# Performance work log

Measured on AMD Instinct MI355X. Metric: run time of the kernel, lower is better.

The kernel has to match this reference:

```python
import jax, jax.numpy as jnp
import numpy as np

# dims
T, B, D = 128, 512, 512          # seq, batch, d_input = dim_aug_state*n_agent
M, H, DH, DFF = 6, 2, 32, 64     # mem_len, heads, d_head_inner, d_ff_inner
ACT = 64                          # dim_action*n_agent
BG = 0.1                          # GRU-gate bias (GTrXL)


def _ln(t, g, b):
    mu = t.mean(-1, keepdims=True)
    var = ((t - mu) ** 2).mean(-1, keepdims=True)
    return (t - mu) / jnp.sqrt(var + 1e-5) * g + b


def _rel_shift(x):
    # x: [T, J, B, H] -> TransformerXL relative shift
    Tq, J = x.shape[0], x.shape[1]
    zp = jnp.zeros((Tq, 1) + x.shape[2:], x.dtype)
    x = jnp.concatenate([zp, x], axis=1)              # [T, J+1, B, H]
    x = x.reshape((J + 1, Tq) + x.shape[2:])[1:]      # [J, T, B, H]
    return x.reshape((Tq, J) + x.shape[2:])


def _gate(x, y, W, b):
    # GRU-style gating g(x, y): x = residual stream, y = new branch output
    lin = lambda t, i: t @ W[i] + b[i]
    r = jax.nn.sigmoid(lin(y, 0) + lin(x, 1))
    z = jax.nn.sigmoid(lin(y, 2) + lin(x, 3) - BG)
    h = jnp.tanh(lin(y, 4) + (r * x) @ W[5] + b[5])
    return (1.0 - z) * x + z * h


def setup_inputs() -> dict:
    key = jax.random.key(0)
    ks = iter(jax.random.split(key, 32))
    rn = lambda shape, s=0.02: jax.random.normal(next(ks), shape, jnp.float32) * s
    return dict(
        aug_states=jax.random.normal(next(ks), (T, B, D), jnp.float32),
        action=jax.random.normal(next(ks), (B, ACT), jnp.float32),
        memory=jnp.zeros((M, B, D), jnp.float32),
        W_q=rn((D, H * DH)), W_kv=rn((D, 2 * H * DH)), W_p=rn((D, H * DH)), W_out=rn((H * DH, D)),
        u=rn((H, DH)), v=rn((H, DH)),
        ln1_g=jnp.ones(D), ln1_b=jnp.zeros(D), ln2_g=jnp.ones(D), ln2_b=jnp.zeros(D),
        ff_W1=rn((D, DFF)), ff_b1=jnp.zeros(DFF), ff_W2=rn((DFF, D)), ff_b2=jnp.zeros(D),
        g1_W=rn((6, D, D)), g1_b=jnp.zeros((6, D)), g2_W=rn((6, D, D)), g2_b=jnp.zeros((6, D)),
        d1_W=rn((D, 1024)), d1_b=jnp.zeros(1024),
        d2_W=rn((1024 + ACT, 512)), d2_b=jnp.zeros(512),
        d3_W=rn((512, 300)), d3_b=jnp.zeros(300),
        d4_W=rn((300, 1)), d4_b=jnp.zeros(1),
    )


def reference(aug_states, action, memory, W_q, W_kv, W_p, W_out, u, v,
              ln1_g, ln1_b, ln2_g, ln2_b, ff_W1, ff_b1, ff_W2, ff_b2,
              g1_W, g1_b, g2_W, g2_b, d1_W, d1_b, d2_W, d2_b, d3_W, d3_b, d4_W, d4_b):
    x = aug_states                                    # [T, B, D]
    J = T + M
    # sinusoidal relative position embeddings for positions J-1 .. 0
    pos = jnp.arange(J - 1, -1, -1.0, dtype=jnp.float32)
    inv_freq = 1.0 / (10000.0 ** (jnp.arange(0, D, 2, dtype=jnp.float32) / D))
    si = pos[:, None] * inv_freq[None, :]
    pos_emb = jnp.concatenate([jnp.sin(si), jnp.cos(si)], axis=-1)   # [J, D]

    # --- stable (pre-LN + gated) TransformerXL layer ---
    src2 = _ln(x, ln1_g, ln1_b)
    cat = jnp.concatenate([memory, src2], axis=0)     # [J, B, D]
    k, vv = jnp.split(cat @ W_kv, 2, axis=-1)
    q = (src2 @ W_q).reshape(T, B, H, DH)
    k = k.reshape(J, B, H, DH)
    vv = vv.reshape(J, B, H, DH)
    p = (pos_emb @ W_p).reshape(J, H, DH)
    content = jnp.einsum("ibhd,jbhd->ijbh", q + u, k)
    position = _rel_shift(jnp.einsum("ibhd,jhd->ijbh", q + v, p))
    attn = content + position                         # [T, J, B, H]
    mask = jnp.arange(J)[None, :] > (jnp.arange(T)[:, None] + M)     # causal w/ memory offset
    attn = jnp.where(mask[:, :, None, None], -jnp.inf, attn)
    attn = jax.nn.softmax(attn * (1.0 / np.sqrt(DH)), axis=1)
    av = jnp.einsum("ijbh,jbhd->ibhd", attn, vv).reshape(T, B, H * DH)
    src = _gate(x, av @ W_out, g1_W, g1_b)
    ff = jax.nn.relu(_ln(src, ln2_g, ln2_b) @ ff_W1 + ff_b1) @ ff_W2 + ff_b2
    out = _gate(src, ff, g2_W, g2_b)                  # [T, B, D]

    # --- mean pool + MLP critic head ---
    ts = out.mean(axis=0)                             # [B, D]
    h1 = jax.nn.relu(ts @ d1_W + d1_b)
    h = jnp.concatenate([h1, action], axis=1)
    h = jax.nn.relu(h @ d2_W + d2_b)
    h = jax.nn.relu(h @ d3_W + d3_b)
    return jax.nn.relu(h @ d4_W + d4_b)               # [B, 1]
```

## Files before the change

### kernel.cpp

```cpp
#include <hip/hip_runtime.h>
#include <math.h>

namespace {

constexpr int kT = 128, kB = 512, kD = 512, kM = 6, kH = 2;
constexpr int kJ = kT + kM;
constexpr float kBG = 0.1f;
constexpr int kTB = kT * kB;
constexpr int kBK = 32;

typedef __attribute__((ext_vector_type(8))) short bf16x8;
typedef __attribute__((ext_vector_type(4))) float f32x4;
typedef __attribute__((ext_vector_type(8))) unsigned short us8;
typedef __attribute__((ext_vector_type(4))) unsigned short us4;

__device__ __forceinline__ float sigmoidf_(float x) {
  return 1.0f / (1.0f + __expf(-x));
}

__device__ __forceinline__ unsigned short bf16u(float f) {
  union { float f; unsigned u; } c; c.f = f;
  unsigned r = c.u + 0x7fffu + ((c.u >> 16) & 1u);
  return (unsigned short)(r >> 16);
}

__device__ __forceinline__ float b2f(unsigned short u) {
  union { unsigned u; float f; } c; c.u = (unsigned)u << 16;
  return c.f;
}

__device__ __forceinline__ void gl_lds16(const void* g, void* l) {
  __builtin_amdgcn_global_load_lds(
      (const __attribute__((address_space(1))) unsigned int*)g,
      (__attribute__((address_space(3))) unsigned int*)l, 16, 0, 0);
}

__global__ __launch_bounds__(256) void transp_kernel(const float* __restrict__ W,
                                                     unsigned short* __restrict__ Wt,
                                                     int K, int N) {
  __shared__ float t[32][33];
  const int n0 = blockIdx.x * 32, k0 = blockIdx.y * 32;
  const float* Wb = W + (size_t)blockIdx.z * K * N;
  unsigned short* Wtb = Wt + (size_t)blockIdx.z * K * N;
  int tx = threadIdx.x & 31, ty = threadIdx.x >> 5;
#pragma unroll
  for (int r = 0; r < 32; r += 8)
    t[ty + r][tx] = Wb[(size_t)(k0 + ty + r) * N + n0 + tx];
  __syncthreads();
#pragma unroll
  for (int r = 0; r < 32; r += 8)
    Wtb[(size_t)(n0 + ty + r) * K + k0 + tx] = bf16u(t[tx][ty + r]);
}

__global__ __launch_bounds__(256) void conv_bf16_kernel(const float* __restrict__ in,
                                                        unsigned short* __restrict__ outb,
                                                        size_t n) {
  size_t idx = ((size_t)blockIdx.x * 256 + threadIdx.x) * 8;
  if (idx >= n) return;
  float4 a = *(const float4*)(in + idx);
  float4 c = *(const float4*)(in + idx + 4);
  us8 o;
  o[0] = bf16u(a.x); o[1] = bf16u(a.y); o[2] = bf16u(a.z); o[3] = bf16u(a.w);
  o[4] = bf16u(c.x); o[5] = bf16u(c.y); o[6] = bf16u(c.z); o[7] = bf16u(c.w);
  *(us8*)(outb + idx) = o;
}

__global__ __launch_bounds__(256) void ln1_dual_kernel(const float* __restrict__ in,
                                                       const float* __restrict__ g,
                                                       const float* __restrict__ b,
                                                       unsigned short* __restrict__ outLN,
                                                       unsigned short* __restrict__ outRaw,
                                                       int nrows) {
  int wave = threadIdx.x >> 6, lane = threadIdx.x & 63;
  int row = blockIdx.x * 4 + wave;
  if (row >= nrows) return;
  const float* p = in + (size_t)row * kD + lane * 8;
  float4 a = *(const float4*)p;
  float4 c = *(const float4*)(p + 4);
  float v[8] = {a.x, a.y, a.z, a.w, c.x, c.y, c.z, c.w};
  float s = 0.f;
#pragma unroll
  for (int i = 0; i < 8; ++i) s += v[i];
#pragma unroll
  for (int off = 32; off; off >>= 1) s += __shfl_xor(s, off);
  float mu = s * (1.0f / 512.0f);
  float q = 0.f;
#pragma unroll
  for (int i = 0; i < 8; ++i) { float d = v[i] - mu; q += d * d; }
#pragma unroll
  for (int off = 32; off; off >>= 1) q += __shfl_xor(q, off);
  float rstd = rsqrtf(q * (1.0f / 512.0f) + 1e-5f);
  us8 oln, oraw;
#pragma unroll
  for (int i = 0; i < 8; ++i) {
    int col = lane * 8 + i;
    oln[i] = bf16u((v[i] - mu) * rstd * g[col] + b[col]);
    oraw[i] = bf16u(v[i]);
  }
  size_t off8 = (size_t)row * kD + lane * 8;
  *(us8*)(outLN + off8) = oln;
  *(us8*)(outRaw + off8) = oraw;
}

__global__ __launch_bounds__(256) void ln_b16_kernel(const unsigned short* __restrict__ in,
                                                     const float* __restrict__ g,
                                                     const float* __restrict__ b,
                                                     unsigned short* __restrict__ outb,
                                                     int nrows) {
  int wave = threadIdx.x >> 6, lane = threadIdx.x & 63;
  int row = blockIdx.x * 4 + wave;
  if (row >= nrows) return;
  us8 iv = *(const us8*)(in + (size_t)row * kD + lane * 8);
  float v[8];
#pragma unroll
  for (int i = 0; i < 8; ++i) v[i] = b2f(iv[i]);
  float s = 0.f;
#pragma unroll
  for (int i = 0; i < 8; ++i) s += v[i];
#pragma unroll
  for (int off = 32; off; off >>= 1) s += __shfl_xor(s, off);
  float mu = s * (1.0f / 512.0f);
  float q = 0.f;
#pragma unroll
  for (int i = 0; i < 8; ++i) { float d = v[i] - mu; q += d * d; }
#pragma unroll
  for (int off = 32; off; off >>= 1) q += __shfl_xor(q, off);
  float rstd = rsqrtf(q * (1.0f / 512.0f) + 1e-5f);
  us8 o;
#pragma unroll
  for (int i = 0; i < 8; ++i) {
    int col = lane * 8 + i;
    o[i] = bf16u((v[i] - mu) * rstd * g[col] + b[col]);
  }
  *(us8*)(outb + (size_t)row * kD + lane * 8) = o;
}

template <int TN, int EPI>
__global__ __launch_bounds__(256) void mfma_gemm_bt(
    const unsigned short* __restrict__ A, const unsigned short* __restrict__ Bt,
    int K, const float* __restrict__ bias, void* __restrict__ Cv, int N) {
  constexpr int MI = (TN == 128) ? 4 : 2;
  constexpr int NJ = 4;
  constexpr int BCH = TN * 64 / 1024;
  __shared__ __align__(16) unsigned short As[128 * kBK];
  __shared__ __align__(16) unsigned short Bs[TN * kBK];
  const int tid = threadIdx.x;
  const int lane = tid & 63, wv = tid >> 6;
  const int ml = lane & 15, qd = lane >> 4;
  const int m0 = blockIdx.y * 128, n0 = blockIdx.x * TN;
  const int mw0 = (TN == 128) ? (wv >> 1) * 64 : wv * 32;
  const int nw0 = (TN == 128) ? (wv & 1) * 64 : 0;
  const size_t ldA = (size_t)K * 2, ldB = (size_t)K * 2;
  const char* Ab = (const char*)A + (size_t)m0 * ldA;
  const char* Bb = (const char*)Bt + (size_t)n0 * ldB;
  f32x4 acc[MI][NJ];
#pragma unroll
  for (int i = 0; i < MI; ++i)
#pragma unroll
    for (int j = 0; j < NJ; ++j) acc[i][j] = (f32x4)0.f;
  for (int k0 = 0; k0 < K; k0 += kBK) {
#pragma unroll
    for (int c = wv; c < 8; c += 4) {
      int fb = c * 1024 + lane * 16;
      gl_lds16(Ab + (size_t)(fb >> 6) * ldA + (fb & 63) + (size_t)k0 * 2,
               (char*)As + c * 1024);
    }
#pragma unroll
    for (int c = wv; c < BCH; c += 4) {
      int fb = c * 1024 + lane * 16;
      gl_lds16(Bb + (size_t)(fb >> 6) * ldB + (fb & 63) + (size_t)k0 * 2,
               (char*)Bs + c * 1024);
    }
    __syncthreads();
    bf16x8 af[MI], bfr[NJ];
#pragma unroll
    for (int i = 0; i < MI; ++i)
      af[i] = *(const bf16x8*)(As + (mw0 + i * 16 + ml) * kBK + qd * 8);
#pragma unroll
    for (int j = 0; j < NJ; ++j)
      bfr[j] = *(const bf16x8*)(Bs + (nw0 + j * 16 + ml) * kBK + qd * 8);
#pragma unroll
    for (int i = 0; i < MI; ++i)
#pragma unroll
      for (int j = 0; j < NJ; ++j)
        acc[i][j] = __builtin_amdgcn_mfma_f32_16x16x32_bf16(af[i], bfr[j], acc[i][j], 0, 0, 0);
    __syncthreads();
  }
#pragma unroll
  for (int i = 0; i < MI; ++i)
#pragma unroll
    for (int j = 0; j < NJ; ++j)
#pragma unroll
      for (int r = 0; r < 4; ++r) {
        int m = m0 + mw0 + i * 16 + qd * 4 + r;
        int n = n0 + nw0 + j * 16 + ml;
        float val = acc[i][j][r];
        if (EPI >= 2) val += bias[n];
        if (EPI == 2) val = fmaxf(val, 0.f);
        size_t idx = (size_t)m * N + n;
        if (EPI == 0) ((float*)Cv)[idx] = val;
        else ((unsigned short*)Cv)[idx] = bf16u(val);
      }
}

template <int NBLOG>
__device__ __forceinline__ void xcd_decode(int& m0, int& n0, int tileN) {
  const int L = blockIdx.x;
  const int xcd = L & 7;
  const int s = L >> 3;
  const int mgPerX = (int)(gridDim.x >> (3 + NBLOG));
  const int mg = xcd * mgPerX + (s >> NBLOG);
  const int nb = s & ((1 << NBLOG) - 1);
  m0 = mg * 128;
  n0 = nb * tileN;
}

__global__ __launch_bounds__(512, 4) void mfma_gate_r(
    const unsigned short* __restrict__ Yb, const unsigned short* __restrict__ Xb,
    const unsigned short* __restrict__ Wt, const float* __restrict__ gb,
    unsigned short* __restrict__ RX) {
  __shared__ __align__(16) unsigned short As[128 * kBK];
  __shared__ __align__(16) unsigned short Bs[256 * kBK];
  const int tid = threadIdx.x;
  const int lane = tid & 63, wv = tid >> 6;
  const int ml = lane & 15, qd = lane >> 4;
  int m0, n0;
  xcd_decode<1>(m0, n0, 256);
  const int mw0 = (wv & 1) * 64, nw0 = (wv >> 1) * 64;
  const size_t ld = (size_t)kD * 2;
  f32x4 acc[4][4];
#pragma unroll
  for (int i = 0; i < 4; ++i)
#pragma unroll
    for (int j = 0; j < 4; ++j) acc[i][j] = (f32x4)0.f;
  for (int p = 0; p < 2; ++p) {
    const char* Ab = (const char*)(p ? Xb : Yb) + (size_t)m0 * ld;
    const char* Bb = (const char*)(Wt + (size_t)p * kD * kD) + (size_t)n0 * ld;
    for (int k0 = 0; k0 < kD; k0 += kBK) {
      {
        int fb = wv * 1024 + lane * 16;
        gl_lds16(Ab + (size_t)(fb >> 6) * ld + (fb & 63) + (size_t)k0 * 2,
                 (char*)As + wv * 1024);
      }
#pragma unroll
      for (int c = wv; c < 16; c += 8) {
        int fb = c * 1024 + lane * 16;
        gl_lds16(Bb + (size_t)(fb >> 6) * ld + (fb & 63) + (size_t)k0 * 2,
                 (char*)Bs + c * 1024);
      }
      __syncthreads();
      bf16x8 af[4], bfr[4];
#pragma unroll
      for (int i = 0; i < 4; ++i)
        af[i] = *(const bf16x8*)(As + (mw0 + i * 16 + ml) * kBK + qd * 8);
#pragma unroll
      for (int j = 0; j < 4; ++j)
        bfr[j] = *(const bf16x8*)(Bs + (nw0 + j * 16 + ml) * kBK + qd * 8);
#pragma unroll
      for (int i = 0; i < 4; ++i)
#pragma unroll
        for (int j = 0; j < 4; ++j)
          acc[i][j] = __builtin_amdgcn_mfma_f32_16x16x32_bf16(af[i], bfr[j], acc[i][j], 0, 0, 0);
      __syncthreads();
    }
  }
#pragma unroll
  for (int i = 0; i < 4; ++i)
#pragma unroll
    for (int j = 0; j < 4; ++j)
#pragma unroll
      for (int r = 0; r < 4; ++r) {
        int m = m0 + mw0 + i * 16 + qd * 4 + r;
        int n = n0 + nw0 + j * 16 + ml;
        float rg = sigmoidf_(acc[i][j][r] + gb[n] + gb[kD + n]);
        size_t idx = (size_t)m * kD + n;
        RX[idx] = bf16u(rg * b2f(Xb[idx]));
      }
}

template <bool POOL>
__global__ __launch_bounds__(512, 4) void mfma_gate_hz(
    const unsigned short* __restrict__ Yb, const unsigned short* __restrict__ RXb,
    const unsigned short* __restrict__ Xb, const unsigned short* __restrict__ Wt,
    const float* __restrict__ gb, unsigned short* __restrict__ OUTb,
    float* __restrict__ TS, int rowoff) {
  __shared__ __align__(16) unsigned short As[128 * kBK];
  __shared__ __align__(16) unsigned short Bs[128 * kBK];
  const int tid = threadIdx.x;
  const int lane = tid & 63, wv = tid >> 6;
  const int ml = lane & 15, qd = lane >> 4;
  int m0, n0;
  xcd_decode<2>(m0, n0, 128);
  const int mw0 = (wv & 3) * 32, nw0 = (wv >> 2) * 64;
  const size_t ld = (size_t)kD * 2;
  const size_t DD = (size_t)kD * kD;
  f32x4 accH[2][4], accZ[2][4];
#pragma unroll
  for (int i = 0; i < 2; ++i)
#pragma unroll
    for (int j = 0; j < 4; ++j) { accH[i][j] = (f32x4)0.f; accZ[i][j] = (f32x4)0.f; }
  const unsigned short* Ap[4] = {Yb, RXb, Yb, Xb};
  const int wsel[4] = {4, 5, 2, 3};
  for (int p = 0; p < 4; ++p) {
    const char* Ab = (const char*)Ap[p] + (size_t)m0 * ld;
    const char* Bb = (const char*)(Wt + (size_t)wsel[p] * DD) + (size_t)n0 * ld;
    f32x4 (*acc)[4] = (p < 2) ? accH : accZ;
    for (int k0 = 0; k0 < kD; k0 += kBK) {
      {
        int fb = wv * 1024 + lane * 16;
        size_t go = (size_t)(fb >> 6) * ld + (fb & 63) + (size_t)k0 * 2;
        gl_lds16(Ab + go, (char*)As + wv * 1024);
        gl_lds16(Bb + go, (char*)Bs + wv * 1024);
      }
      __syncthreads();
      bf16x8 af[2], bfr[4];
#pragma unroll
      for (int i = 0; i < 2; ++i)
        af[i] = *(const bf16x8*)(As + (mw0 + i * 16 + ml) * kBK + qd * 8);
#pragma unroll
      for (int j = 0; j < 4; ++j)
        bfr[j] = *(const bf16x8*)(Bs + (nw0 + j * 16 + ml) * kBK + qd * 8);
#pragma unroll
      for (int i = 0; i < 2; ++i)
#pragma unroll
        for (int j = 0; j < 4; ++j)
          acc[i][j] = __builtin_amdgcn_mfma_f32_16x16x32_bf16(af[i], bfr[j], acc[i][j], 0, 0, 0);
      __syncthreads();
    }
  }
#pragma unroll
  for (int i = 0; i < 2; ++i)
#pragma unroll
    for (int j = 0; j < 4; ++j)
#pragma unroll
      for (int r = 0; r < 4; ++r) {
        int m = m0 + mw0 + i * 16 + qd * 4 + r;
        int n = n0 + nw0 + j * 16 + ml;
        float z = sigmoidf_(accZ[i][j][r] + gb[2 * kD + n] + gb[3 * kD + n] - kBG);
        float hc = tanhf(accH[i][j][r] + gb[4 * kD + n] + gb[5 * kD + n]);
        size_t idx = (size_t)m * kD + n;
        float val = (1.0f - z) * b2f(Xb[idx]) + z * hc;
        if (POOL) {
          int b = (rowoff + m) & (kB - 1);
          atomicAdd(TS + (size_t)b * kD + n, val * (1.0f / kT));
        } else {
          OUTb[idx] = bf16u(val);
        }
      }
}

__global__ __launch_bounds__(64) void posp_kernel(const float* __restrict__ Wp,
                                                  float* __restrict__ P) {
  __shared__ float emb[512];
  int jj = blockIdx.x;
  int t = threadIdx.x;
  float pos = (float)(kJ - 1 - jj);
#pragma unroll
  for (int r = 0; r < 8; ++r) {
    int d = t + r * 64;
    int i = (d < 256) ? d : d - 256;
    float invf = expf(-((float)(2 * i) * (1.0f / 512.0f)) * 9.210340371976184f);
    float si = pos * invf;
    emb[d] = (d < 256) ? sinf(si) : cosf(si);
  }
  __syncthreads();
  float acc = 0.f;
  for (int d = 0; d < 512; ++d) acc = fmaf(emb[d], Wp[d * 64 + t], acc);
  P[jj * 64 + t] = acc;
}

__global__ __launch_bounds__(128) void attn_kernel(
    const float* __restrict__ Q, const unsigned short* __restrict__ KV,
    const float* __restrict__ P, const float* __restrict__ U,
    const float* __restrict__ V, unsigned short* __restrict__ AV) {
  __shared__ float ks[kJ][32];
  __shared__ float vs[kJ][32];
  __shared__ float ps[32][kJ + 2];
  const int b = blockIdx.x, h = blockIdx.y;
  const int tid = threadIdx.x;
  for (int idx = tid; idx < kJ * 8; idx += 128) {
    int j = idx >> 3, seg = idx & 7;
    const unsigned short* src = KV + ((size_t)(j * kB + b)) * 128 + h * 32 + seg * 4;
    us4 kq = *(const us4*)src;
    us4 vq = *(const us4*)(src + 64);
#pragma unroll
    for (int e = 0; e < 4; ++e) {
      ks[j][seg * 4 + e] = b2f(kq[e]);
      vs[j][seg * 4 + e] = b2f(vq[e]);
    }
  }
  for (int idx = tid; idx < kJ * 8; idx += 128) {
    int j = idx >> 3, seg = idx & 7;
    float4 pq = *(const float4*)(P + j * 64 + h * 32 + seg * 4);
    ps[seg * 4 + 0][j] = pq.x;
    ps[seg * 4 + 1][j] = pq.y;
    ps[seg * 4 + 2][j] = pq.z;
    ps[seg * 4 + 3][j] = pq.w;
  }
  __syncthreads();
  const int i = tid;
  float qu[32], qv[32];
  const float* qp = Q + ((size_t)(i * kB + b)) * 64 + h * 32;
#pragma unroll
  for (int d = 0; d < 32; ++d) {
    float qd = qp[d];
    qu[d] = qd + U[h * 32 + d];
    qv[d] = qd + V[h * 32 + d];
  }
  float m = -INFINITY, l = 0.f, acc[32] = {};
  const float scale = 0.17677669529663687f;
  for (int j = 0; j <= i + kM; ++j) {
    float s = 0.f;
#pragma unroll
    for (int d = 0; d < 32; d += 4) {
      float4 k4 = *(const float4*)&ks[j][d];
      s = fmaf(qu[d + 0], k4.x, s);
      s = fmaf(qu[d + 1], k4.y, s);
      s = fmaf(qu[d + 2], k4.z, s);
      s = fmaf(qu[d + 3], k4.w, s);
    }
    int jj = j + (kT - 1) - i;
#pragma unroll
    for (int d = 0; d < 32; ++d) s = fmaf(qv[d], ps[d][jj], s);
    float ls = s * scale;
    float nm = fmaxf(m, ls);
    float w = __expf(ls - nm);
    float f = __expf(m - nm);
    l = l * f + w;
#pragma unroll
    for (int d = 0; d < 32; d += 4) {
      float4 v4 = *(const float4*)&vs[j][d];
      acc[d + 0] = fmaf(acc[d + 0], f, w * v4.x);
      acc[d + 1] = fmaf(acc[d + 1], f, w * v4.y);
      acc[d + 2] = fmaf(acc[d + 2], f, w * v4.z);
      acc[d + 3] = fmaf(acc[d + 3], f, w * v4.w);
    }
    m = nm;
  }
  float inv = 1.0f / l;
  unsigned short* o = AV + ((size_t)(i * kB + b)) * 64 + h * 32;
#pragma unroll
  for (int d = 0; d < 32; ++d) o[d] = bf16u(acc[d] * inv);
}

template <int ACTF, bool DUAL>
__global__ __launch_bounds__(256) void gemm_kernel(
    const float* __restrict__ A1, const float* __restrict__ Bm1, int K1,
    const float* __restrict__ A2, const float* __restrict__ Bm2, int K2,
    const float* __restrict__ bias, float* __restrict__ C, int Mrows, int N) {
  __shared__ float As[16][68];
  __shared__ float Bs[16][68];
  const int tid = threadIdx.x;
  const int tx = tid & 15, ty = tid >> 4;
  const int m0 = blockIdx.y * 64, n0 = blockIdx.x * 64;
  const int ar = tid >> 2, aseg = tid & 3;
  float acc[4][4] = {};
#pragma unroll
  for (int pass = 0; pass < (DUAL ? 2 : 1); ++pass) {
    const float* A = (DUAL && pass) ? A2 : A1;
    const float* Bm = (DUAL && pass) ? Bm2 : Bm1;
    const int K = (DUAL && pass) ? K2 : K1;
    for (int k0 = 0; k0 < K; k0 += 16) {
      {
        int row = m0 + ar;
        int kb = k0 + aseg * 4;
        float x0 = 0.f, x1 = 0.f, x2 = 0.f, x3 = 0.f;
        if (row < Mrows) {
          const float* ap = A + (size_t)row * K + kb;
          if (kb + 3 < K) {
            float4 t = *(const float4*)ap;
            x0 = t.x; x1 = t.y; x2 = t.z; x3 = t.w;
          } else {
            if (kb + 0 < K) x0 = ap[0];
            if (kb + 1 < K) x1 = ap[1];
            if (kb + 2 < K) x2 = ap[2];
          }
        }
        As[aseg * 4 + 0][ar] = x0;
        As[aseg * 4 + 1][ar] = x1;
        As[aseg * 4 + 2][ar] = x2;
        As[aseg * 4 + 3][ar] = x3;
      }
      {
        int krow = k0 + ty;
        int nb = n0 + tx * 4;
        float y0 = 0.f, y1 = 0.f, y2 = 0.f, y3 = 0.f;
        if (krow < K) {
          const float* bp = Bm + (size_t)krow * N + nb;
          if (nb + 3 < N) {
            float4 t = *(const float4*)bp;
            y0 = t.x; y1 = t.y; y2 = t.z; y3 = t.w;
          } else {
            if (nb + 0 < N) y0 = bp[0];
            if (nb + 1 < N) y1 = bp[1];
            if (nb + 2 < N) y2 = bp[2];
          }
        }
        *(float4*)&Bs[ty][tx * 4] = make_float4(y0, y1, y2, y3);
      }
      __syncthreads();
#pragma unroll
      for (int kk = 0; kk < 16; ++kk) {
        float a[4], bb[4];
        *(float4*)a = *(const float4*)&As[kk][ty * 4];
        *(float4*)bb = *(const float4*)&Bs[kk][tx * 4];
#pragma unroll
        for (int i = 0; i < 4; ++i)
#pragma unroll
          for (int j = 0; j < 4; ++j) acc[i][j] = fmaf(a[i], bb[j], acc[i][j]);
      }
      __syncthreads();
    }
  }
#pragma unroll
  for (int i = 0; i < 4; ++i) {
    int m = m0 + ty * 4 + i;
    if (m >= Mrows) continue;
#pragma unroll
    for (int j = 0; j < 4; ++j) {
      int n = n0 + tx * 4 + j;
      if (n >= N) continue;
      float val = acc[i][j];
      if (bias) val += bias[n];
      if (ACTF == 1) val = fmaxf(val, 0.f);
      C[(size_t)m * N + n] = val;
    }
  }
}

}

extern "C" void kernel_launch(void* const* d_in, const int* in_sizes, int n_in,
                              void* d_out, int out_size, void* d_ws, size_t ws_size,
                              hipStream_t stream) {
  (void)in_sizes; (void)n_in; (void)out_size;
  const float* aug    = (const float*)d_in[0];
  const float* action = (const float*)d_in[1];
  const float* memory = (const float*)d_in[2];
  const float* W_q    = (const float*)d_in[3];
  const float* W_kv   = (const float*)d_in[4];
  const float* W_p    = (const float*)d_in[5];
  const float* W_out  = (const float*)d_in[6];
  const float* u      = (const float*)d_in[7];
  const float* v      = (const float*)d_in[8];
  const float* ln1_g  = (const float*)d_in[9];
  const float* ln1_b  = (const float*)d_in[10];
  const float* ln2_g  = (const float*)d_in[11];
  const float* ln2_b  = (const float*)d_in[12];
  const float* ff_W1  = (const float*)d_in[13];
  const float* ff_b1  = (const float*)d_in[14];
  const float* ff_W2  = (const float*)d_in[15];
  const float* ff_b2  = (const float*)d_in[16];
  const float* g1_W   = (const float*)d_in[17];
  const float* g1_b   = (const float*)d_in[18];
  const float* g2_W   = (const float*)d_in[19];
  const float* g2_b   = (const float*)d_in[20];
  const float* d1_W   = (const float*)d_in[21];
  const float* d1_b   = (const float*)d_in[22];
  const float* d2_W   = (const float*)d_in[23];
  const float* d2_b   = (const float*)d_in[24];
  const float* d3_W   = (const float*)d_in[25];
  const float* d3_b   = (const float*)d_in[26];
  const float* d4_W   = (const float*)d_in[27];
  const float* d4_b   = (const float*)d_in[28];
  float* out = (float*)d_out;

  char* base = (char*)d_ws;
  auto alloc = [&](size_t bytes) -> char* {
    char* p = base;
    base += (bytes + 255) & ~(size_t)255;
    return p;
  };
  unsigned short* Wqt  = (unsigned short*)alloc((size_t)64 * 512 * 2);
  unsigned short* Wkvt = (unsigned short*)alloc((size_t)128 * 512 * 2);
  unsigned short* Wot  = (unsigned short*)alloc((size_t)512 * 64 * 2);
  unsigned short* Wf1t = (unsigned short*)alloc((size_t)64 * 512 * 2);
  unsigned short* Wf2t = (unsigned short*)alloc((size_t)512 * 64 * 2);
  unsigned short* G1t  = (unsigned short*)alloc((size_t)6 * 512 * 512 * 2);
  unsigned short* G2t  = (unsigned short*)alloc((size_t)6 * 512 * 512 * 2);
  unsigned short* Memb = (unsigned short*)alloc((size_t)3072 * 512 * 2);
  unsigned short* KVb  = (unsigned short*)alloc((size_t)kJ * kB * 128 * 2);
  float* Qb  = (float*)alloc((size_t)kTB * 64 * 4);
  unsigned short* AVb = (unsigned short*)alloc((size_t)kTB * 64 * 2);
  unsigned short* Xb  = (unsigned short*)alloc((size_t)kTB * kD * 2);
  float* Pb  = (float*)alloc((size_t)kJ * 64 * 4);
  float* TSb = (float*)alloc((size_t)kB * kD * 4);
  float* H1b = (float*)alloc((size_t)kB * 1024 * 4);
  float* H2b = (float*)alloc((size_t)kB * 512 * 4);
  float* H3b = (float*)alloc((size_t)kB * 320 * 4);
  size_t fixedBytes = (size_t)(base - (char*)d_ws);
  const size_t ln1Bytes = (size_t)kTB * kD * 2;
  int nch = 1;
  while (nch < 32) {
    size_t chunkBytes = (size_t)(kTB / nch) * 4224 + 4096;
    size_t reuse = chunkBytes > ln1Bytes ? chunkBytes : ln1Bytes;
    if (fixedBytes + reuse <= ws_size) break;
    nch <<= 1;
  }
  const int CR = kTB / nch;
  char* R = base;
  unsigned short* L1b = (unsigned short*)R;
  char* rp = R;
  auto ralloc = [&](size_t bytes) -> char* {
    char* p = rp;
    rp += (bytes + 255) & ~(size_t)255;
    return p;
  };
  unsigned short* Ycb   = (unsigned short*)ralloc((size_t)CR * 512 * 2);
  unsigned short* RXcb  = (unsigned short*)ralloc((size_t)CR * 512 * 2);
  unsigned short* SRCcb = (unsigned short*)ralloc((size_t)CR * 512 * 2);
  unsigned short* LN2cb = (unsigned short*)ralloc((size_t)CR * 512 * 2);
  unsigned short* F1cb  = (unsigned short*)ralloc((size_t)CR * 64 * 2);

  const float* np = nullptr;
  const int MG = CR / 128;

  hipMemsetAsync(TSb, 0, (size_t)kB * kD * sizeof(float), stream);
  transp_kernel<<<dim3(2, 16, 1), 256, 0, stream>>>(W_q, Wqt, 512, 64);
  transp_kernel<<<dim3(4, 16, 1), 256, 0, stream>>>(W_kv, Wkvt, 512, 128);
  transp_kernel<<<dim3(16, 2, 1), 256, 0, stream>>>(W_out, Wot, 64, 512);
  transp_kernel<<<dim3(2, 16, 1), 256, 0, stream>>>(ff_W1, Wf1t, 512, 64);
  transp_kernel<<<dim3(16, 2, 1), 256, 0, stream>>>(ff_W2, Wf2t, 64, 512);
  transp_kernel<<<dim3(16, 16, 6), 256, 0, stream>>>(g1_W, G1t, 512, 512);
  transp_kernel<<<dim3(16, 16, 6), 256, 0, stream>>>(g2_W, G2t, 512, 512);
  conv_bf16_kernel<<<(3072 * 512 / 8 + 255) / 256, 256, 0, stream>>>(
      memory, Memb, (size_t)3072 * 512);
  ln1_dual_kernel<<<kTB / 4, 256, 0, stream>>>(aug, ln1_g, ln1_b, L1b, Xb, kTB);
  mfma_gemm_bt<128, 1><<<dim3(1, 3072 / 128), 256, 0, stream>>>(
      Memb, Wkvt, 512, np, KVb, 128);
  mfma_gemm_bt<128, 1><<<dim3(1, kTB / 128), 256, 0, stream>>>(
      L1b, Wkvt, 512, np, KVb + (size_t)3072 * 128, 128);
  mfma_gemm_bt<64, 0><<<dim3(1, kTB / 128), 256, 0, stream>>>(
      L1b, Wqt, 512, np, Qb, 64);
  posp_kernel<<<kJ, 64, 0, stream>>>(W_p, Pb);
  attn_kernel<<<dim3(kB, kH), 128, 0, stream>>>(Qb, KVb, Pb, u, v, AVb);

  for (int c = 0; c < nch; ++c) {
    const int R0 = c * CR;
    const unsigned short* Xc = Xb + (size_t)R0 * kD;
    mfma_gemm_bt<128, 1><<<dim3(4, MG), 256, 0, stream>>>(
        AVb + (size_t)R0 * 64, Wot, 64, np, Ycb, 512);
    mfma_gate_r<<<2 * MG, 512, 0, stream>>>(Ycb, Xc, G1t, g1_b, RXcb);
    mfma_gate_hz<false><<<4 * MG, 512, 0, stream>>>(
        Ycb, RXcb, Xc, G1t, g1_b, SRCcb, nullptr, R0);
    ln_b16_kernel<<<CR / 4, 256, 0, stream>>>(SRCcb, ln2_g, ln2_b, LN2cb, CR);
    mfma_gemm_bt<64, 2><<<dim3(1, MG), 256, 0, stream>>>(
        LN2cb, Wf1t, 512, ff_b1, F1cb, 64);
    mfma_gemm_bt<128, 3><<<dim3(4, MG), 256, 0, stream>>>(
        F1cb, Wf2t, 64, ff_b2, Ycb, 512);
    mfma_gate_r<<<2 * MG, 512, 0, stream>>>(Ycb, SRCcb, G2t, g2_b, RXcb);
    mfma_gate_hz<true><<<4 * MG, 512, 0, stream>>>(
        Ycb, RXcb, SRCcb, G2t, g2_b, nullptr, TSb, R0);
  }

  gemm_kernel<1, false><<<dim3(16, kB / 64), 256, 0, stream>>>(
      TSb, d1_W, 512, np, np, 0, d1_b, H1b, kB, 1024);
  gemm_kernel<1, true><<<dim3(8, kB / 64), 256, 0, stream>>>(
      H1b, d2_W, 1024, action, d2_W + (size_t)1024 * 512, 64, d2_b, H2b, kB, 512);
  gemm_kernel<1, false><<<dim3(5, kB / 64), 256, 0, stream>>>(
      H2b, d3_W, 512, np, np, 0, d3_b, H3b, kB, 300);
  gemm_kernel<1, false><<<dim3(1, kB / 64), 256, 0, stream>>>(
      H3b, d4_W, 300, np, np, 0, d4_b, out, kB, 1);
}
```

Baseline: 1.514 ms.

## Move z-gate GEMM into first gate kernel and replace pooling atomics with reduction

The GRU gate's z pre-activation GEMM now runs in the first gate kernel, which also computes the r gate. It uses twice as many blocks, and the z half writes fp32 partials to a new chunk buffer. The second kernel then only does the h GEMM (two K-passes instead of four) with 128x256 tiles. The mean-pool atomics are replaced by writing fp32 outputs and running a separate per-batch reduction kernel. This rebalances GEMM work across kernels and removes atomic contention, at the cost of an extra fp32 round trip through memory and a larger workspace per chunk.

```diff
diff --git a/kernel.cpp b/kernel.cpp
--- a/kernel.cpp
+++ b/kernel.cpp
@@ -215,10 +215,90 @@
   n0 = nb * tileN;
 }
 
-__global__ __launch_bounds__(512, 4) void mfma_gate_r(
+__global__ __launch_bounds__(512, 4) void mfma_gate_a(
     const unsigned short* __restrict__ Yb, const unsigned short* __restrict__ Xb,
     const unsigned short* __restrict__ Wt, const float* __restrict__ gb,
-    unsigned short* __restrict__ RX) {
+    unsigned short* __restrict__ RX, float* __restrict__ Zp) {
+  __shared__ __align__(16) unsigned short As[128 * kBK];
+  __shared__ __align__(16) unsigned short Bs[256 * kBK];
+  const int tid = threadIdx.x;
+  const int lane = tid & 63, wv = tid >> 6;
+  const int ml = lane & 15, qd = lane >> 4;
+  int m0, n0;
+  xcd_decode<2>(m0, n0, 256);
+  const int nhalf = n0 >> 9;
+  const int n0e = n0 & 511;
+  const int mw0 = (wv & 1) * 64, nw0 = (wv >> 1) * 64;
+  const size_t ld = (size_t)kD * 2;
+  const size_t DD = (size_t)kD * kD;
+  f32x4 acc[4][4];
+#pragma unroll
+  for (int i = 0; i < 4; ++i)
+#pragma unroll
+    for (int j = 0; j < 4; ++j) acc[i][j] = (f32x4)0.f;
+  for (int p = 0; p < 2; ++p) {
+    const char* Ab = (const char*)(p ? Xb : Yb) + (size_t)m0 * ld;
+    const char* Bb = (const char*)(Wt + (size_t)(2 * nhalf + p) * DD) + (size_t)n0e * ld;
+    for (int k0 = 0; k0 < kD; k0 += kBK) {
+      {
+        int fb = wv * 1024 + lane * 16;
+        gl_lds16(Ab + (size_t)(fb >> 6) * ld + (fb & 63) + (size_t)k0 * 2,
+                 (char*)As + wv * 1024);
+      }
+#pragma unroll
+      for (int c = wv; c < 16; c += 8) {
+        int fb = c * 1024 + lane * 16;
+        gl_lds16(Bb + (size_t)(fb >> 6) * ld + (fb & 63) + (size_t)k0 * 2,
+                 (char*)Bs + c * 1024);
+      }
+      __syncthreads();
+      bf16x8 af[4], bfr[4];
+#pragma unroll
+      for (int i = 0; i < 4; ++i)
+        af[i] = *(const bf16x8*)(As + (mw0 + i * 16 + ml) * kBK + qd * 8);
+#pragma unroll
+      for (int j = 0; j < 4; ++j)
+        bfr[j] = *(const bf16x8*)(Bs + (nw0 + j * 16 + ml) * kBK + qd * 8);
+#pragma unroll
+      for (int i = 0; i < 4; ++i)
+#pragma unroll
+        for (int j = 0; j < 4; ++j)
+          acc[i][j] = __builtin_amdgcn_mfma_f32_16x16x32_bf16(af[i], bfr[j], acc[i][j], 0, 0, 0);
+      __syncthreads();
+    }
+  }
+  if (nhalf == 0) {
+#pragma unroll
+    for (int i = 0; i < 4; ++i)
+#pragma unroll
+      for (int j = 0; j < 4; ++j)
+#pragma unroll
+        for (int r = 0; r < 4; ++r) {
+          int m = m0 + mw0 + i * 16 + qd * 4 + r;
+          int n = n0e + nw0 + j * 16 + ml;
+          float rg = sigmoidf_(acc[i][j][r] + gb[n] + gb[kD + n]);
+          size_t idx = (size_t)m * kD + n;
+          RX[idx] = bf16u(rg * b2f(Xb[idx]));
+        }
+  } else {
+#pragma unroll
+    for (int i = 0; i < 4; ++i)
+#pragma unroll
+      for (int j = 0; j < 4; ++j)
+#pragma unroll
+        for (int r = 0; r < 4; ++r) {
+          int m = m0 + mw0 + i * 16 + qd * 4 + r;
+          int n = n0e + nw0 + j * 16 + ml;
+          Zp[(size_t)m * kD + n] = acc[i][j][r];
+        }
+  }
+}
+
+template <bool POOL>
+__global__ __launch_bounds__(512, 4) void mfma_gate_b(
+    const unsigned short* __restrict__ Yb, const unsigned short* __restrict__ RXb,
+    const unsigned short* __restrict__ Xb, const unsigned short* __restrict__ Wt,
+    const float* __restrict__ gb, float* Zp, unsigned short* __restrict__ OUTb) {
   __shared__ __align__(16) unsigned short As[128 * kBK];
   __shared__ __align__(16) unsigned short Bs[256 * kBK];
   const int tid = threadIdx.x;
@@ -228,14 +308,15 @@
   xcd_decode<1>(m0, n0, 256);
   const int mw0 = (wv & 1) * 64, nw0 = (wv >> 1) * 64;
   const size_t ld = (size_t)kD * 2;
+  const size_t DD = (size_t)kD * kD;
   f32x4 acc[4][4];
 #pragma unroll
   for (int i = 0; i < 4; ++i)
 #pragma unroll
     for (int j = 0; j < 4; ++j) acc[i][j] = (f32x4)0.f;
   for (int p = 0; p < 2; ++p) {
-    const char* Ab = (const char*)(p ? Xb : Yb) + (size_t)m0 * ld;
-    const char* Bb = (const char*)(Wt + (size_t)p * kD * kD) + (size_t)n0 * ld;
+    const char* Ab = (const char*)(p ? RXb : Yb) + (size_t)m0 * ld;
+    const char* Bb = (const char*)(Wt + (size_t)(4 + p) * DD) + (size_t)n0 * ld;
     for (int k0 = 0; k0 < kD; k0 += kBK) {
       {
         int fb = wv * 1024 + lane * 16;
@@ -272,81 +353,35 @@
       for (int r = 0; r < 4; ++r) {
         int m = m0 + mw0 + i * 16 + qd * 4 + r;
         int n = n0 + nw0 + j * 16 + ml;
-        float rg = sigmoidf_(acc[i][j][r] + gb[n] + gb[kD + n]);
         size_t idx = (size_t)m * kD + n;
-        RX[idx] = bf16u(rg * b2f(Xb[idx]));
-      }
-}
-
-template <bool POOL>
-__global__ __launch_bounds__(512, 4) void mfma_gate_hz(
-    const unsigned short* __restrict__ Yb, const unsigned short* __restrict__ RXb,
-    const unsigned short* __restrict__ Xb, const unsigned short* __restrict__ Wt,
-    const float* __restrict__ gb, unsigned short* __restrict__ OUTb,
-    float* __restrict__ TS, int rowoff) {
-  __shared__ __align__(16) unsigned short As[128 * kBK];
-  __shared__ __align__(16) unsigned short Bs[128 * kBK];
-  const int tid = threadIdx.x;
-  const int lane = tid & 63, wv = tid >> 6;
-  const int ml = lane & 15, qd = lane >> 4;
-  int m0, n0;
-  xcd_decode<2>(m0, n0, 128);
-  const int mw0 = (wv & 3) * 32, nw0 = (wv >> 2) * 64;
-  const size_t ld = (size_t)kD * 2;
-  const size_t DD = (size_t)kD * kD;
-  f32x4 accH[2][4], accZ[2][4];
-#pragma unroll
-  for (int i = 0; i < 2; ++i)
-#pragma unroll
-    for (int j = 0; j < 4; ++j) { accH[i][j] = (f32x4)0.f; accZ[i][j] = (f32x4)0.f; }
-  const unsigned short* Ap[4] = {Yb, RXb, Yb, Xb};
-  const int wsel[4] = {4, 5, 2, 3};
-  for (int p = 0; p < 4; ++p) {
-    const char* Ab = (const char*)Ap[p] + (size_t)m0 * ld;
-    const char* Bb = (const char*)(Wt + (size_t)wsel[p] * DD) + (size_t)n0 * ld;
-    f32x4 (*acc)[4] = (p < 2) ? accH : accZ;
-    for (int k0 = 0; k0 < kD; k0 += kBK) {
-      {
-        int fb = wv * 1024 + lane * 16;
-        size_t go = (size_t)(fb >> 6) * ld + (fb & 63) + (size_t)k0 * 2;
-        gl_lds16(Ab + go, (char*)As + wv * 1024);
-        gl_lds16(Bb + go, (char*)Bs + wv * 1024);
-      }
-      __syncthreads();
-      bf16x8 af[2], bfr[4];
-#pragma unroll
-      for (int i = 0; i < 2; ++i)
-        af[i] = *(const bf16x8*)(As + (mw0 + i * 16 + ml) * kBK + qd * 8);
-#pragma unroll
-      for (int j = 0; j < 4; ++j)
-        bfr[j] = *(const bf16x8*)(Bs + (nw0 + j * 16 + ml) * kBK + qd * 8);
-#pragma unroll
-      for (int i = 0; i < 2; ++i)
-#pragma unroll
-        for (int j = 0; j < 4; ++j)
-          acc[i][j] = __builtin_amdgcn_mfma_f32_16x16x32_bf16(af[i], bfr[j], acc[i][j], 0, 0, 0);
-      __syncthreads();
-    }
-  }
-#pragma unroll
-  for (int i = 0; i < 2; ++i)
-#pragma unroll
-    for (int j = 0; j < 4; ++j)
-#pragma unroll
-      for (int r = 0; r < 4; ++r) {
-        int m = m0 + mw0 + i * 16 + qd * 4 + r;
-        int n = n0 + nw0 + j * 16 + ml;
-        float z = sigmoidf_(accZ[i][j][r] + gb[2 * kD + n] + gb[3 * kD + n] - kBG);
-        float hc = tanhf(accH[i][j][r] + gb[4 * kD + n] + gb[5 * kD + n]);
-        size_t idx = (size_t)m * kD + n;
+        float z = sigmoidf_(Zp[idx] + gb[2 * kD + n] + gb[3 * kD + n] - kBG);
+        float hc = tanhf(acc[i][j][r] + gb[4 * kD + n] + gb[5 * kD + n]);
         float val = (1.0f - z) * b2f(Xb[idx]) + z * hc;
-        if (POOL) {
-          int b = (rowoff + m) & (kB - 1);
-          atomicAdd(TS + (size_t)b * kD + n, val * (1.0f / kT));
-        } else {
-          OUTb[idx] = bf16u(val);
-        }
-      }
+        if (POOL) Zp[idx] = val;
+        else OUTb[idx] = bf16u(val);
+      }
+}
+
+__global__ __launch_bounds__(256) void pool_kernel(const float* __restrict__ OUT,
+                                                   float* __restrict__ TS, int Tc) {
+  __shared__ float sh[4][512];
+  const int b = blockIdx.x;
+  const int w = threadIdx.x >> 6, l = threadIdx.x & 63;
+  float acc[8] = {};
+  for (int t = w; t < Tc; t += 4) {
+    const float* p = OUT + ((size_t)t * 512 + b) * 512 + l * 8;
+    float4 a = *(const float4*)p;
+    float4 c = *(const float4*)(p + 4);
+    acc[0] += a.x; acc[1] += a.y; acc[2] += a.z; acc[3] += a.w;
+    acc[4] += c.x; acc[5] += c.y; acc[6] += c.z; acc[7] += c.w;
+  }
+#pragma unroll
+  for (int i = 0; i < 8; ++i) sh[w][l * 8 + i] = acc[i];
+  __syncthreads();
+  for (int n = threadIdx.x; n < 512; n += 256) {
+    TS[(size_t)b * 512 + n] +=
+        (sh[0][n] + sh[1][n] + sh[2][n] + sh[3][n]) * (1.0f / (float)kT);
+  }
 }
 
 __global__ __launch_bounds__(64) void posp_kernel(const float* __restrict__ Wp,
@@ -592,7 +627,7 @@
   const size_t ln1Bytes = (size_t)kTB * kD * 2;
   int nch = 1;
   while (nch < 32) {
-    size_t chunkBytes = (size_t)(kTB / nch) * 4224 + 4096;
+    size_t chunkBytes = (size_t)(kTB / nch) * 6272 + 4096;
     size_t reuse = chunkBytes > ln1Bytes ? chunkBytes : ln1Bytes;
     if (fixedBytes + reuse <= ws_size) break;
     nch <<= 1;
@@ -611,6 +646,7 @@
   unsigned short* SRCcb = (unsigned short*)ralloc((size_t)CR * 512 * 2);
   unsigned short* LN2cb = (unsigned short*)ralloc((size_t)CR * 512 * 2);
   unsigned short* F1cb  = (unsigned short*)ralloc((size_t)CR * 64 * 2);
+  float* Zpb            = (float*)ralloc((size_t)CR * 512 * 4);
 
   const float* np = nullptr;
   const int MG = CR / 128;
@@ -640,17 +676,18 @@
     const unsigned short* Xc = Xb + (size_t)R0 * kD;
     mfma_gemm_bt<128, 1><<<dim3(4, MG), 256, 0, stream>>>(
         AVb + (size_t)R0 * 64, Wot, 64, np, Ycb, 512);
-    mfma_gate_r<<<2 * MG, 512, 0, stream>>>(Ycb, Xc, G1t, g1_b, RXcb);
-    mfma_gate_hz<false><<<4 * MG, 512, 0, stream>>>(
-        Ycb, RXcb, Xc, G1t, g1_b, SRCcb, nullptr, R0);
+    mfma_gate_a<<<MG * 4, 512, 0, stream>>>(Ycb, Xc, G1t, g1_b, RXcb, Zpb);
+    mfma_gate_b<false><<<MG * 2, 512, 0, stream>>>(
+        Ycb, RXcb, Xc, G1t, g1_b, Zpb, SRCcb);
     ln_b16_kernel<<<CR / 4, 256, 0, stream>>>(SRCcb, ln2_g, ln2_b, LN2cb, CR);
     mfma_gemm_bt<64, 2><<<dim3(1, MG), 256, 0, stream>>>(
         LN2cb, Wf1t, 512, ff_b1, F1cb, 64);
     mfma_gemm_bt<128, 3><<<dim3(4, MG), 256, 0, stream>>>(
         F1cb, Wf2t, 64, ff_b2, Ycb, 512);
-    mfma_gate_r<<<2 * MG, 512, 0, stream>>>(Ycb, SRCcb, G2t, g2_b, RXcb);
-    mfma_gate_hz<true><<<4 * MG, 512, 0, stream>>>(
-        Ycb, RXcb, SRCcb, G2t, g2_b, nullptr, TSb, R0);
+    mfma_gate_a<<<MG * 4, 512, 0, stream>>>(Ycb, SRCcb, G2t, g2_b, RXcb, Zpb);
+    mfma_gate_b<true><<<MG * 2, 512, 0, stream>>>(
+        Ycb, RXcb, SRCcb, G2t, g2_b, Zpb, nullptr);
+    pool_kernel<<<kB, 256, 0, stream>>>(Zpb, TSb, CR / 512);
   }
 
   gemm_kernel<1, false><<<dim3(16, kB / 64), 256, 0, stream>>>(
```

New measurement: 1.683 ms. +11.2%, slower.
